# Performance work log

Measured on AMD Instinct MI355X. Metric: run time of the kernel, lower is better.

The kernel has to match this reference:

```python
import jax, jax.numpy as jnp
import numpy as np

N_CELLS = 8_388_608   # total flattened cells across all subdomains (~4096x2048 global grid)
N_HALO = 1_048_576    # total halo (boundary) destination cells across all subdomain edges
N_Q = 12              # raw field quantities: u, v, b_u, b_v, h, H, hh, dif_h, eta1, k_u, k_v, k3


def setup_inputs() -> dict:
    key = jax.random.key(0)
    k1, k2, k3 = jax.random.split(key, 3)
    fields = jax.random.normal(k1, (N_Q, N_CELLS), dtype=jnp.float32)
    # precomputed gather map: each halo cell reads up to 2 source cells
    src_idx = jax.random.randint(k2, (N_HALO, 2), 0, N_CELLS, dtype=jnp.int32)
    # ratio map: coarse->fine (ratio 0.5, repeat_interleave) = copy [1,0];
    # fine->coarse (ratio 2, mean over group of 2) = [0.5,0.5]; ratio 1 = copy [1,0]
    coarse = jax.random.bernoulli(k3, 0.5, (N_HALO,))
    weights = jnp.where(coarse[:, None],
                        jnp.array([0.5, 0.5], dtype=jnp.float32),
                        jnp.array([1.0, 0.0], dtype=jnp.float32))
    return {"fields": fields, "src_idx": src_idx, "weights": weights}


def reference(fields, src_idx, weights):
    # unpack raw quantities
    u, v, b_u, b_v, h, Hb, hh, dif_h, eta1, k_u, k_v, k3 = fields
    # derived boundary quantities exchanged by update_halos (11 halo buffers)
    derived = jnp.stack([
        u, v, b_u, b_v, h, hh, dif_h,
        h + Hb,                    # halo_eta
        eta1,                      # halo_eta1
        jnp.minimum(k_u, k3),      # halo_k_uu
        jnp.minimum(k_v, k3),      # halo_k_vv
    ])  # [11, N_CELLS]
    # batched gather-rescale-scatter: halo[q, e] = sum_j weights[e, j] * derived[q, src_idx[e, j]]
    gathered = derived[:, src_idx]                     # [11, E, 2]
    halos = jnp.einsum('qej,ej->qe', gathered, weights)  # [11, E]
    return halos
```

## Files before the change

### kernel.cpp

```cpp
#include <hip/hip_runtime.h>

#define N_CELLS 8388608
#define N_HALO  1048576
#define STRIDE  16

__global__ __launch_bounds__(256) void pack_kernel(
    const float* __restrict__ fields, float* __restrict__ ws)
{
    const int c = blockIdx.x * blockDim.x + threadIdx.x;
    if (c >= N_CELLS) return;

    float f[12];
    #pragma unroll
    for (int q = 0; q < 12; ++q)
        f[q] = fields[(size_t)q * N_CELLS + c];

    float4* o = (float4*)(ws + (size_t)c * STRIDE);
    o[0] = make_float4(f[0], f[1], f[2], f[3]);
    o[1] = make_float4(f[4], f[6], f[7], f[4] + f[5]);
    o[2] = make_float4(f[8], fminf(f[9], f[11]), fminf(f[10], f[11]), 0.0f);
    o[3] = make_float4(0.0f, 0.0f, 0.0f, 0.0f);
}

__global__ __launch_bounds__(256) void gather_kernel(
    const float* __restrict__ ws, const int2* __restrict__ src_idx,
    const float2* __restrict__ weights, float* __restrict__ out)
{
    const int e = blockIdx.x * blockDim.x + threadIdx.x;
    if (e >= N_HALO) return;

    const int2   ij = src_idx[e];
    const float2 wv = weights[e];

    const float4* p0 = (const float4*)(ws + (size_t)ij.x * STRIDE);
    float4 a0 = p0[0], a1 = p0[1], a2 = p0[2];

    float4 b0 = make_float4(0,0,0,0), b1 = b0, b2 = b0;
    if (wv.y != 0.0f) {
        const float4* p1 = (const float4*)(ws + (size_t)ij.y * STRIDE);
        b0 = p1[0]; b1 = p1[1]; b2 = p1[2];
    }

    const float w0 = wv.x, w1 = wv.y;
    out[0ull*N_HALO + e]  = a0.x*w0 + b0.x*w1;
    out[1ull*N_HALO + e]  = a0.y*w0 + b0.y*w1;
    out[2ull*N_HALO + e]  = a0.z*w0 + b0.z*w1;
    out[3ull*N_HALO + e]  = a0.w*w0 + b0.w*w1;
    out[4ull*N_HALO + e]  = a1.x*w0 + b1.x*w1;
    out[5ull*N_HALO + e]  = a1.y*w0 + b1.y*w1;
    out[6ull*N_HALO + e]  = a1.z*w0 + b1.z*w1;
    out[7ull*N_HALO + e]  = a1.w*w0 + b1.w*w1;
    out[8ull*N_HALO + e]  = a2.x*w0 + b2.x*w1;
    out[9ull*N_HALO + e]  = a2.y*w0 + b2.y*w1;
    out[10ull*N_HALO + e] = a2.z*w0 + b2.z*w1;
}

extern "C" void kernel_launch(void* const* d_in, const int* in_sizes, int n_in,
                              void* d_out, int out_size, void* d_ws, size_t ws_size,
                              hipStream_t stream) {
    const float*  fields  = (const float*)d_in[0];
    const int2*   src_idx = (const int2*)d_in[1];
    const float2* weights = (const float2*)d_in[2];
    float* out = (float*)d_out;
    float* ws  = (float*)d_ws;

    const int block = 256;
    pack_kernel  <<<(N_CELLS + block - 1) / block, block, 0, stream>>>(fields, ws);
    gather_kernel<<<(N_HALO  + block - 1) / block, block, 0, stream>>>(ws, src_idx, weights, out);
}
```

Before: 759.3 us.

## Drop full-grid pack pass; gather directly from raw fields in phased blocks

Removes the pack kernel, which read all 12 fields over every cell and wrote a 64-byte-stride workspace, even though only about 1M halo cells times 2 sources are ever read. A single kernel now gathers straight from the raw field arrays and computes the derived quantities (h+H, min) on the fly. The grid is split into five phases by block index, each handling a few quantities, so the working set of each phase stays small and cache friendly. Outputs use nontemporal stores. The trade-off is more scattered 4-byte random reads in place of 64-byte row reads, and src_idx and weights are reloaded once per phase.

Result: no change. 749.6 us (-1.3%).

```diff
diff --git a/kernel.cpp b/kernel.cpp
--- a/kernel.cpp
+++ b/kernel.cpp
@@ -2,57 +2,76 @@
 
 #define N_CELLS 8388608
 #define N_HALO  1048576
-#define STRIDE  16
 
-__global__ __launch_bounds__(256) void pack_kernel(
-    const float* __restrict__ fields, float* __restrict__ ws)
-{
-    const int c = blockIdx.x * blockDim.x + threadIdx.x;
-    if (c >= N_CELLS) return;
-
-    float f[12];
-    #pragma unroll
-    for (int q = 0; q < 12; ++q)
-        f[q] = fields[(size_t)q * N_CELLS + c];
-
-    float4* o = (float4*)(ws + (size_t)c * STRIDE);
-    o[0] = make_float4(f[0], f[1], f[2], f[3]);
-    o[1] = make_float4(f[4], f[6], f[7], f[4] + f[5]);
-    o[2] = make_float4(f[8], fminf(f[9], f[11]), fminf(f[10], f[11]), 0.0f);
-    o[3] = make_float4(0.0f, 0.0f, 0.0f, 0.0f);
-}
-
-__global__ __launch_bounds__(256) void gather_kernel(
-    const float* __restrict__ ws, const int2* __restrict__ src_idx,
+__global__ __launch_bounds__(256) void halo_gather(
+    const float* __restrict__ fields, const int2* __restrict__ src_idx,
     const float2* __restrict__ weights, float* __restrict__ out)
 {
-    const int e = blockIdx.x * blockDim.x + threadIdx.x;
-    if (e >= N_HALO) return;
+    const int bid   = blockIdx.x;
+    const int phase = bid >> 12;
+    const int e     = ((bid & 4095) << 8) | threadIdx.x;
 
-    const int2   ij = src_idx[e];
-    const float2 wv = weights[e];
+    const int2   ij  = src_idx[e];
+    const float2 wv  = weights[e];
+    const float  w0  = wv.x, w1 = wv.y;
+    const bool   two = (w1 != 0.0f);
+    const size_t ix  = (size_t)ij.x, iy = (size_t)ij.y;
 
-    const float4* p0 = (const float4*)(ws + (size_t)ij.x * STRIDE);
-    float4 a0 = p0[0], a1 = p0[1], a2 = p0[2];
-
-    float4 b0 = make_float4(0,0,0,0), b1 = b0, b2 = b0;
-    if (wv.y != 0.0f) {
-        const float4* p1 = (const float4*)(ws + (size_t)ij.y * STRIDE);
-        b0 = p1[0]; b1 = p1[1]; b2 = p1[2];
+    switch (phase) {
+    case 0: {
+        const float* r0 = fields + 0ull * N_CELLS;
+        const float* r1 = fields + 1ull * N_CELLS;
+        float o0 = r0[ix] * w0, o1 = r1[ix] * w0;
+        if (two) { o0 += r0[iy] * w1; o1 += r1[iy] * w1; }
+        __builtin_nontemporal_store(o0, out + 0ull * N_HALO + e);
+        __builtin_nontemporal_store(o1, out + 1ull * N_HALO + e);
+        break; }
+    case 1: {
+        const float* r2 = fields + 2ull * N_CELLS;
+        const float* r3 = fields + 3ull * N_CELLS;
+        float o2 = r2[ix] * w0, o3 = r3[ix] * w0;
+        if (two) { o2 += r2[iy] * w1; o3 += r3[iy] * w1; }
+        __builtin_nontemporal_store(o2, out + 2ull * N_HALO + e);
+        __builtin_nontemporal_store(o3, out + 3ull * N_HALO + e);
+        break; }
+    case 2: {
+        const float* r4 = fields + 4ull * N_CELLS;
+        const float* r5 = fields + 5ull * N_CELLS;
+        float ha = r4[ix], hba = r5[ix];
+        float o4 = ha * w0, o7 = (ha + hba) * w0;
+        if (two) {
+            float hb = r4[iy], hbb = r5[iy];
+            o4 += hb * w1; o7 += (hb + hbb) * w1;
+        }
+        __builtin_nontemporal_store(o4, out + 4ull * N_HALO + e);
+        __builtin_nontemporal_store(o7, out + 7ull * N_HALO + e);
+        break; }
+    case 3: {
+        const float* r6 = fields + 6ull * N_CELLS;
+        const float* r7 = fields + 7ull * N_CELLS;
+        const float* r8 = fields + 8ull * N_CELLS;
+        float o5 = r6[ix] * w0, o6 = r7[ix] * w0, o8 = r8[ix] * w0;
+        if (two) { o5 += r6[iy] * w1; o6 += r7[iy] * w1; o8 += r8[iy] * w1; }
+        __builtin_nontemporal_store(o5, out + 5ull * N_HALO + e);
+        __builtin_nontemporal_store(o6, out + 6ull * N_HALO + e);
+        __builtin_nontemporal_store(o8, out + 8ull * N_HALO + e);
+        break; }
+    default: {
+        const float* r9  = fields +  9ull * N_CELLS;
+        const float* r10 = fields + 10ull * N_CELLS;
+        const float* r11 = fields + 11ull * N_CELLS;
+        float kua = r9[ix], kva = r10[ix], k3a = r11[ix];
+        float o9  = fminf(kua, k3a) * w0;
+        float o10 = fminf(kva, k3a) * w0;
+        if (two) {
+            float kub = r9[iy], kvb = r10[iy], k3b = r11[iy];
+            o9  += fminf(kub, k3b) * w1;
+            o10 += fminf(kvb, k3b) * w1;
+        }
+        __builtin_nontemporal_store(o9,  out +  9ull * N_HALO + e);
+        __builtin_nontemporal_store(o10, out + 10ull * N_HALO + e);
+        break; }
     }
-
-    const float w0 = wv.x, w1 = wv.y;
-    out[0ull*N_HALO + e]  = a0.x*w0 + b0.x*w1;
-    out[1ull*N_HALO + e]  = a0.y*w0 + b0.y*w1;
-    out[2ull*N_HALO + e]  = a0.z*w0 + b0.z*w1;
-    out[3ull*N_HALO + e]  = a0.w*w0 + b0.w*w1;
-    out[4ull*N_HALO + e]  = a1.x*w0 + b1.x*w1;
-    out[5ull*N_HALO + e]  = a1.y*w0 + b1.y*w1;
-    out[6ull*N_HALO + e]  = a1.z*w0 + b1.z*w1;
-    out[7ull*N_HALO + e]  = a1.w*w0 + b1.w*w1;
-    out[8ull*N_HALO + e]  = a2.x*w0 + b2.x*w1;
-    out[9ull*N_HALO + e]  = a2.y*w0 + b2.y*w1;
-    out[10ull*N_HALO + e] = a2.z*w0 + b2.z*w1;
 }
 
 extern "C" void kernel_launch(void* const* d_in, const int* in_sizes, int n_in,
@@ -62,9 +81,7 @@
     const int2*   src_idx = (const int2*)d_in[1];
     const float2* weights = (const float2*)d_in[2];
     float* out = (float*)d_out;
-    float* ws  = (float*)d_ws;
+    (void)d_ws; (void)ws_size;
 
-    const int block = 256;
-    pack_kernel  <<<(N_CELLS + block - 1) / block, block, 0, stream>>>(fields, ws);
-    gather_kernel<<<(N_HALO  + block - 1) / block, block, 0, stream>>>(ws, src_idx, weights, out);
+    halo_gather<<<5 * (N_HALO / 256), 256, 0, stream>>>(fields, src_idx, weights, out);
 }
```
